# Kernel tuning notes

Hardware: AMD Instinct MI355X
Metric: run time of the kernel (lower is better)

Reference implementation:

```python
import jax, jax.numpy as jnp
import numpy as np

H, HKV, D, HID, INT = 16, 4, 128, 2048, 8192
ROPE_THETA = 10000.0
EPS = 1e-6
NEG = -1e30


def rmsnorm(x, w):
    v = jnp.mean(x * x, axis=-1, keepdims=True)
    return x * jax.lax.rsqrt(v + EPS) * w


def apply_rope(t, pos):
    # t: [B,S,h,D], pos: [S]
    half = D // 2
    inv_freq = 1.0 / (ROPE_THETA ** (jnp.arange(0, half, dtype=jnp.float32) / half))
    ang = pos.astype(jnp.float32)[:, None] * inv_freq  # [S, D/2]
    cos = jnp.cos(ang)[None, :, None, :]
    sin = jnp.sin(ang)[None, :, None, :]
    t1, t2 = t[..., :half], t[..., half:]
    return jnp.concatenate([t1 * cos - t2 * sin, t2 * cos + t1 * sin], axis=-1)


def setup_inputs() -> dict:
    key = jax.random.key(0)
    ks = jax.random.split(key, 5)
    B, S = 4, 1024
    s = 0.02  # init scale for weights
    return {
        "x": jax.random.normal(ks[0], (B, S, HID), jnp.float32),
        "ln1_w": jnp.ones((HID,), jnp.float32),
        "wqkv": jax.random.normal(ks[1], (HID, (H + 2 * HKV) * D), jnp.float32) * s,
        "wo": jax.random.normal(ks[2], (H * D, HID), jnp.float32) * s,
        "ln2_w": jnp.ones((HID,), jnp.float32),
        "w_gate_up": jax.random.normal(ks[3], (HID, 2 * INT), jnp.float32) * s,
        "w_down": jax.random.normal(ks[4], (INT, HID), jnp.float32) * s,
        "pos": jnp.arange(S, dtype=jnp.int32),
    }


def reference(x, ln1_w, wqkv, wo, ln2_w, w_gate_up, w_down, pos):
    B, S, _ = x.shape
    # --- attention block (prefill paged attention == dense causal attention) ---
    h = rmsnorm(x, ln1_w)
    qkv = h @ wqkv  # [B,S,(H+2*HKV)*D]
    q = qkv[..., : H * D].reshape(B, S, H, D)
    k = qkv[..., H * D : (H + HKV) * D].reshape(B, S, HKV, D)
    v = qkv[..., (H + HKV) * D :].reshape(B, S, HKV, D)
    q = apply_rope(q, pos)
    k = apply_rope(k, pos)
    g = H // HKV  # GQA group size
    k = jnp.repeat(k, g, axis=2)
    v = jnp.repeat(v, g, axis=2)
    scores = jnp.einsum("bqhd,bkhd->bhqk", q, k) / np.float32(np.sqrt(D))
    causal = pos[:, None] >= pos[None, :]  # [S,S]
    scores = jnp.where(causal[None, None], scores, NEG)
    attn = jax.nn.softmax(scores, axis=-1)
    o = jnp.einsum("bhqk,bkhd->bqhd", attn, v).reshape(B, S, H * D) @ wo
    h1 = x + o
    # --- SwiGLU MLP block ---
    gu = rmsnorm(h1, ln2_w) @ w_gate_up
    gate, up = gu[..., :INT], gu[..., INT:]
    return h1 + (jax.nn.silu(gate) * up) @ w_down
```

## Files before the change

### kernel.cpp

```cpp
#include <hip/hip_runtime.h>
#include <math.h>

#define B_    4
#define S_    1024
#define H_    16
#define HKV_  4
#define D_    128
#define HID_  2048
#define INT_  8192
#define QKVD_ 3072
#define NTOK_ 4096
#define NEG_  -1.0e30f

typedef unsigned short u16;
typedef unsigned int   u32;
typedef float  f32x4  __attribute__((ext_vector_type(4)));
typedef __bf16 bf16x8 __attribute__((ext_vector_type(8)));

__device__ __forceinline__ float bf2f(u16 v) {
    union { u32 u; float f; } c; c.u = ((u32)v) << 16; return c.f;
}
__device__ __forceinline__ u16 f2bf(float f) {
    union { float f; u32 u; } c; c.f = f;
    return (u16)((c.u + 0x7fffu + ((c.u >> 16) & 1u)) >> 16);
}

__device__ __forceinline__ void async_ld16(const u16* g, u16* l) {
    __builtin_amdgcn_global_load_lds(
        (const __attribute__((address_space(1))) void*)g,
        (__attribute__((address_space(3))) void*)l, 16, 0, 0);
}

__device__ __forceinline__ int swz_col(int e) {
    return ((((e >> 3) & 3) ^ ((e >> 5) & 3) ^ ((e >> 7) & 3)) << 3);
}

__device__ __forceinline__ void xcd2d(int gx, int gy, int RX, int RY,
                                      int& bx, int& by) {
    const int f = by * gx + bx;
    const int xcd = f & 7, slot = f >> 3;
    const int wx = gx / RX, wy = gy / RY;
    const int rx = xcd % RX, ry = xcd / RX;
    bx = rx * wx + (slot % wx);
    by = ry * wy + (slot / wx);
}

__global__ void detect_k(const u16* __restrict__ w, int* __restrict__ flag) {
    if (threadIdx.x == 0) *flag = (w[0] == 0x3F80u) ? 0 : 1;
}

__global__ void cvt_x_k(const void* __restrict__ in, const int* __restrict__ flag,
                        u16* __restrict__ out) {
    int i = blockIdx.x * 256 + threadIdx.x;
    if (*flag == 0) {
        ((ushort4*)out)[i] = ((const ushort4*)in)[i];
    } else {
        float4 v = ((const float4*)in)[i];
        ushort4 o;
        o.x = f2bf(v.x); o.y = f2bf(v.y); o.z = f2bf(v.z); o.w = f2bf(v.w);
        ((ushort4*)out)[i] = o;
    }
}

__global__ void cvt_w_k(const void* __restrict__ in, const int* __restrict__ flag,
                        float* __restrict__ out, int n) {
    int i = blockIdx.x * 256 + threadIdx.x;
    if (i < n) out[i] = (*flag == 0) ? bf2f(((const u16*)in)[i]) : ((const float*)in)[i];
}

__global__ void transpose_k(const void* __restrict__ in, const int* __restrict__ flag,
                            u16* __restrict__ out, int K, int N) {
    __shared__ u16 t[64][65];
    const bool isf32 = (*flag != 0);
    int tx = blockIdx.x * 64;
    int ty = blockIdx.y * 64;
    const int c4 = (threadIdx.x & 15) * 4;
    const int r0 = threadIdx.x >> 4;
    for (int r = r0; r < 64; r += 16) {
        size_t idx = (size_t)(ty + r) * N + tx + c4;
        if (isf32) {
            float4 v = *(const float4*)((const float*)in + idx);
            t[c4 + 0][r] = f2bf(v.x); t[c4 + 1][r] = f2bf(v.y);
            t[c4 + 2][r] = f2bf(v.z); t[c4 + 3][r] = f2bf(v.w);
        } else {
            ushort4 v = *(const ushort4*)((const u16*)in + idx);
            t[c4 + 0][r] = v.x; t[c4 + 1][r] = v.y;
            t[c4 + 2][r] = v.z; t[c4 + 3][r] = v.w;
        }
    }
    __syncthreads();
    for (int i = threadIdx.x; i < 64 * 16; i += 256) {
        int r = i >> 4, c = (i & 15) * 4;
        ushort4 v;
        v.x = t[r][c]; v.y = t[r][c + 1]; v.z = t[r][c + 2]; v.w = t[r][c + 3];
        *(ushort4*)(out + (size_t)(tx + r) * K + ty + c) = v;
    }
}

__global__ void rmsnorm_k(const u16* __restrict__ x, const float* __restrict__ w,
                          u16* __restrict__ y) {
    int row = blockIdx.x;
    const u16* xr = x + (size_t)row * HID_;
    u16* yr = y + (size_t)row * HID_;
    int t = threadIdx.x;
    u16 xs[8];
    *(uint4*)xs = ((const uint4*)xr)[t];
    float v[8]; float ss = 0.f;
    #pragma unroll
    for (int i = 0; i < 8; i++) { v[i] = bf2f(xs[i]); ss += v[i] * v[i]; }
    #pragma unroll
    for (int o = 32; o > 0; o >>= 1) ss += __shfl_down(ss, o, 64);
    __shared__ float wsum[4];
    if ((t & 63) == 0) wsum[t >> 6] = ss;
    __syncthreads();
    float tot = wsum[0] + wsum[1] + wsum[2] + wsum[3];
    float scale = rsqrtf(tot * (1.0f / HID_) + 1e-6f);
    float4 w0 = ((const float4*)w)[t * 2];
    float4 w1 = ((const float4*)w)[t * 2 + 1];
    float wf[8] = {w0.x, w0.y, w0.z, w0.w, w1.x, w1.y, w1.z, w1.w};
    u16 ys[8];
    #pragma unroll
    for (int i = 0; i < 8; i++) ys[i] = f2bf(v[i] * scale * wf[i]);
    ((uint4*)yr)[t] = *(uint4*)ys;
}

__global__ void rope_table_k(const int* __restrict__ pos,
                             float* __restrict__ cosT, float* __restrict__ sinT) {
    int s = blockIdx.x;
    int d = threadIdx.x;
    double inv = exp(-((double)d / 64.0) * 9.210340371976184);
    double ang = (double)pos[s] * inv;
    cosT[s * 64 + d] = (float)cos(ang);
    sinT[s * 64 + d] = (float)sin(ang);
}

__global__ void rope_apply_k(u16* __restrict__ qkv, const float* __restrict__ cosT,
                             const float* __restrict__ sinT) {
    int id = blockIdx.x * 256 + threadIdx.x;
    int d4 = (id & 15) * 4;
    int rest = id >> 4;
    int head = rest % 20;
    int bs = rest / 20;
    int s = bs & (S_ - 1);
    size_t base = (size_t)bs * QKVD_ + head * D_;
    ushort4 lo = *(ushort4*)(qkv + base + d4);
    ushort4 hi = *(ushort4*)(qkv + base + 64 + d4);
    float4 c  = *(const float4*)(cosT + s * 64 + d4);
    float4 sn = *(const float4*)(sinT + s * 64 + d4);
    float t1[4] = {bf2f(lo.x), bf2f(lo.y), bf2f(lo.z), bf2f(lo.w)};
    float t2[4] = {bf2f(hi.x), bf2f(hi.y), bf2f(hi.z), bf2f(hi.w)};
    float cf[4] = {c.x, c.y, c.z, c.w};
    float sf[4] = {sn.x, sn.y, sn.z, sn.w};
    ushort4 olo, ohi;
    olo.x = f2bf(t1[0] * cf[0] - t2[0] * sf[0]);
    olo.y = f2bf(t1[1] * cf[1] - t2[1] * sf[1]);
    olo.z = f2bf(t1[2] * cf[2] - t2[2] * sf[2]);
    olo.w = f2bf(t1[3] * cf[3] - t2[3] * sf[3]);
    ohi.x = f2bf(t2[0] * cf[0] + t1[0] * sf[0]);
    ohi.y = f2bf(t2[1] * cf[1] + t1[1] * sf[1]);
    ohi.z = f2bf(t2[2] * cf[2] + t1[2] * sf[2]);
    ohi.w = f2bf(t2[3] * cf[3] + t1[3] * sf[3]);
    *(ushort4*)(qkv + base + d4)      = olo;
    *(ushort4*)(qkv + base + 64 + d4) = ohi;
}

template<int EPI>
__global__ __launch_bounds__(512, 2) void gemm256_k(
    const u16* __restrict__ A, const u16* __restrict__ Bt,
    void* __restrict__ Cv, int M, int N, int K, int RX, int RY)
{
    __shared__ __align__(16) u16 lds[3 * 16384];

    int bx = blockIdx.x, by = blockIdx.y;
    xcd2d(gridDim.x, gridDim.y, RX, RY, bx, by);

    const int tid  = threadIdx.x;
    const int m0 = by * 256, n0 = bx * 256;
    const int wave = tid >> 6, lane = tid & 63;
    const int wmi = wave >> 2, wni = wave & 3;
    const int r16 = lane & 15, quad = lane >> 4;

    const int NT = K >> 5;

    auto stageA = [&](int bufi, int tt) {
        u16* dst = lds + bufi * 16384;
        const size_t gb = (size_t)m0 * K + (size_t)tt * 32;
        #pragma unroll
        for (int rr = 0; rr < 2; ++rr) {
            const int e = rr * 4096 + tid * 8;
            async_ld16(A + gb + (size_t)(e >> 5) * K + swz_col(e), dst + e);
        }
    };
    auto stageB = [&](int bufi, int tt) {
        u16* dst = lds + bufi * 16384 + 8192;
        const size_t gb = (size_t)n0 * K + (size_t)tt * 32;
        #pragma unroll
        for (int rr = 0; rr < 2; ++rr) {
            const int e = rr * 4096 + tid * 8;
            async_ld16(Bt + gb + (size_t)(e >> 5) * K + swz_col(e), dst + e);
        }
    };

    f32x4 acc[8][4] = {};

    stageA(0, 0); stageB(0, 0);
    stageA(1, 1); stageB(1, 1);
    asm volatile("s_waitcnt vmcnt(4)" ::: "memory");
    __builtin_amdgcn_s_barrier();

    const int gsw = quad ^ (r16 & 3) ^ ((r16 >> 2) & 3);
    const int aoff = wmi * 4096 + r16 * 32 + gsw * 8;
    const int boff = 8192 + wni * 2048 + r16 * 32 + gsw * 8;

    for (int t = 0; t < NT; ++t) {
        const u16* buf = lds + (t % 3) * 16384;
        const int nb = (t + 2) % 3;
        const bool pf = (t + 2) < NT;
        bf16x8 a[4], b[4], a2[4];
        #pragma unroll
        for (int i = 0; i < 4; ++i) a[i] = *(const bf16x8*)(buf + aoff + i * 512);
        #pragma unroll
        for (int j = 0; j < 4; ++j) b[j] = *(const bf16x8*)(buf + boff + j * 512);
        if (pf) stageA(nb, t + 2);
        __builtin_amdgcn_s_barrier();
        asm volatile("s_waitcnt lgkmcnt(0)" ::: "memory");
        __builtin_amdgcn_sched_barrier(0);
        __builtin_amdgcn_s_setprio(1);
        #pragma unroll
        for (int i = 0; i < 4; ++i)
            #pragma unroll
            for (int j = 0; j < 4; ++j)
                acc[i][j] = __builtin_amdgcn_mfma_f32_16x16x32_bf16(a[i], b[j], acc[i][j], 0, 0, 0);
        __builtin_amdgcn_s_setprio(0);
        __builtin_amdgcn_s_barrier();
        #pragma unroll
        for (int i = 0; i < 4; ++i) a2[i] = *(const bf16x8*)(buf + aoff + (i + 4) * 512);
        if (pf) stageB(nb, t + 2);
        __builtin_amdgcn_s_barrier();
        asm volatile("s_waitcnt lgkmcnt(0)" ::: "memory");
        __builtin_amdgcn_sched_barrier(0);
        __builtin_amdgcn_s_setprio(1);
        #pragma unroll
        for (int i = 0; i < 4; ++i)
            #pragma unroll
            for (int j = 0; j < 4; ++j)
                acc[i + 4][j] = __builtin_amdgcn_mfma_f32_16x16x32_bf16(a2[i], b[j], acc[i + 4][j], 0, 0, 0);
        __builtin_amdgcn_s_setprio(0);
        if (t == NT - 2) { asm volatile("s_waitcnt vmcnt(0)" ::: "memory"); }
        else             { asm volatile("s_waitcnt vmcnt(4)" ::: "memory"); }
        __builtin_amdgcn_s_barrier();
    }

    u16* C16 = (u16*)Cv;
    #pragma unroll
    for (int i = 0; i < 8; ++i) {
        const int mb = m0 + wmi * 128 + i * 16 + quad * 4;
        #pragma unroll
        for (int j = 0; j < 4; ++j) {
            const int n = n0 + wni * 64 + j * 16 + r16;
            #pragma unroll
            for (int r = 0; r < 4; ++r) {
                size_t idx = (size_t)(mb + r) * N + n;
                float v = acc[i][j][r];
                if (EPI == 2) { v = v / (1.f + __expf(-v)); v *= bf2f(C16[idx]); }
                C16[idx] = f2bf(v);
            }
        }
    }
}

template<int EPI>
__global__ __launch_bounds__(512, 2) void gemm_bt2_k(
    const u16* __restrict__ A, const u16* __restrict__ Bt,
    void* __restrict__ Cv, const u16* __restrict__ R,
    const int* __restrict__ flag, int M, int N, int K, int RX, int RY)
{
    __shared__ __align__(16) u16 lds[3 * 12288];

    int bx = blockIdx.x, by = blockIdx.y;
    xcd2d(gridDim.x, gridDim.y, RX, RY, bx, by);

    const int tid  = threadIdx.x;
    const int m0 = by * 128, n0 = bx * 256;
    const int wave = tid >> 6, lane = tid & 63;
    const int wmi = wave >> 2, wni = wave & 3;
    const int r16 = lane & 15, quad = lane >> 4;

    const int NT = K >> 5;

    auto stageA = [&](int bufi, int tt) {
        u16* dst = lds + bufi * 12288;
        const size_t gb = (size_t)m0 * K + (size_t)tt * 32;
        const int e = tid * 8;
        async_ld16(A + gb + (size_t)(e >> 5) * K + swz_col(e), dst + e);
    };
    auto stageB = [&](int bufi, int tt) {
        u16* dst = lds + bufi * 12288 + 4096;
        const size_t gb = (size_t)n0 * K + (size_t)tt * 32;
        #pragma unroll
        for (int rr = 0; rr < 2; ++rr) {
            const int e = rr * 4096 + tid * 8;
            async_ld16(Bt + gb + (size_t)(e >> 5) * K + swz_col(e), dst + e);
        }
    };

    f32x4 acc[4][4] = {};

    stageA(0, 0); stageB(0, 0);
    stageA(1, 1); stageB(1, 1);
    asm volatile("s_waitcnt vmcnt(3)" ::: "memory");
    __builtin_amdgcn_s_barrier();

    const int gsw = quad ^ (r16 & 3) ^ ((r16 >> 2) & 3);
    const int aoff = wmi * 2048 + r16 * 32 + gsw * 8;
    const int boff = 4096 + wni * 2048 + r16 * 32 + gsw * 8;

    for (int t = 0; t < NT; ++t) {
        const u16* buf = lds + (t % 3) * 12288;
        const int nb = (t + 2) % 3;
        const bool pf = (t + 2) < NT;
        bf16x8 a[4], b2[2], b3[2];
        #pragma unroll
        for (int i = 0; i < 4; ++i) a[i] = *(const bf16x8*)(buf + aoff + i * 512);
        #pragma unroll
        for (int j = 0; j < 2; ++j) b2[j] = *(const bf16x8*)(buf + boff + j * 512);
        if (pf) stageA(nb, t + 2);
        __builtin_amdgcn_s_barrier();
        asm volatile("s_waitcnt lgkmcnt(0)" ::: "memory");
        __builtin_amdgcn_sched_barrier(0);
        __builtin_amdgcn_s_setprio(1);
        #pragma unroll
        for (int i = 0; i < 4; ++i)
            #pragma unroll
            for (int j = 0; j < 2; ++j)
                acc[i][j] = __builtin_amdgcn_mfma_f32_16x16x32_bf16(a[i], b2[j], acc[i][j], 0, 0, 0);
        __builtin_amdgcn_s_setprio(0);
        __builtin_amdgcn_s_barrier();
        #pragma unroll
        for (int j = 0; j < 2; ++j) b3[j] = *(const bf16x8*)(buf + boff + (j + 2) * 512);
        if (pf) stageB(nb, t + 2);
        __builtin_amdgcn_s_barrier();
        asm volatile("s_waitcnt lgkmcnt(0)" ::: "memory");
        __builtin_amdgcn_sched_barrier(0);
        __builtin_amdgcn_s_setprio(1);
        #pragma unroll
        for (int i = 0; i < 4; ++i)
            #pragma unroll
            for (int j = 0; j < 2; ++j)
                acc[i][j + 2] = __builtin_amdgcn_mfma_f32_16x16x32_bf16(a[i], b3[j], acc[i][j + 2], 0, 0, 0);
        __builtin_amdgcn_s_setprio(0);
        if (t == NT - 2) { asm volatile("s_waitcnt vmcnt(0)" ::: "memory"); }
        else             { asm volatile("s_waitcnt vmcnt(3)" ::: "memory"); }
        __builtin_amdgcn_s_barrier();
    }

    u16* C16 = (u16*)Cv;
    float* C32 = (float*)Cv;
    bool f32out = false;
    if (EPI == 3) f32out = (*flag != 0);

    #pragma unroll
    for (int i = 0; i < 4; ++i) {
        const int mb = m0 + wmi * 64 + i * 16 + quad * 4;
        #pragma unroll
        for (int j = 0; j < 4; ++j) {
            const int n = n0 + wni * 64 + j * 16 + r16;
            #pragma unroll
            for (int r = 0; r < 4; ++r) {
                size_t idx = (size_t)(mb + r) * N + n;
                float v = acc[i][j][r];
                v += bf2f(R[idx]);
                if (EPI == 3 && f32out) C32[idx] = v;
                else C16[idx] = f2bf(v);
            }
        }
    }
}

__global__ __launch_bounds__(256) void attn_mfma_k(
    const u16* __restrict__ qkv, u16* __restrict__ out)
{
    __shared__ __align__(16) u16 Vt[128 * 136];
    __shared__ __align__(16) u16 Ps[64 * 136];

    int bswz_x, bswz_y, bswz_z;
    {
        const int orig = blockIdx.x + (S_ / 64) * (blockIdx.y + H_ * blockIdx.z);
        const int q = ((S_ / 64) * H_ * B_) >> 3;
        const int wg = (orig & 7) * q + (orig >> 3);
        bswz_x = wg & (S_ / 64 - 1);
        bswz_y = (wg >> 4) & (H_ - 1);
        bswz_z = wg >> 8;
    }

    const int tid  = threadIdx.x;
    const int wave = tid >> 6, lane = tid & 63;
    const int r16  = lane & 15, quad = lane >> 4;
    const int q0 = bswz_x * 64;
    const int h  = bswz_y;
    const int b  = bswz_z;
    const int kh = h >> 2;
    const float scale = 0.08838834764831845f;

    bf16x8 a_q[4];
    {
        const u16* qp = qkv + ((size_t)(b * S_ + q0 + wave * 16 + r16) * QKVD_ + h * D_ + quad * 8);
        #pragma unroll
        for (int ks = 0; ks < 4; ks++)
            a_q[ks] = *(const bf16x8*)(qp + ks * 32);
    }

    float mrun[4], lrun[4];
    #pragma unroll
    for (int r = 0; r < 4; r++) { mrun[r] = -3.0e38f; lrun[r] = 0.f; }
    f32x4 acc_o[8] = {};
    const int myrow_c = q0 + wave * 16 + quad * 4;

    const int ntiles = (q0 >> 7) + 1;
    for (int kt = 0; kt < ntiles; kt++) {
        const int j0 = kt * 128;
        __syncthreads();
        {
            const int key = tid & 127, dh = (tid >> 7) * 64;
            const u16* vp = qkv + ((size_t)(b * S_ + j0 + key) * QKVD_ + (H_ + HKV_ + kh) * D_ + dh);
            #pragma unroll
            for (int i = 0; i < 8; i++) {
                u16 tmp[8];
                *(uint4*)tmp = *(const uint4*)(vp + i * 8);
                #pragma unroll
                for (int j = 0; j < 8; j++)
                    Vt[(dh + i * 8 + j) * 136 + key] = tmp[j];
            }
        }
        f32x4 acc_s[8] = {};
        __builtin_amdgcn_s_setprio(1);
        #pragma unroll
        for (int ks = 0; ks < 4; ks++) {
            #pragma unroll
            for (int nt = 0; nt < 8; nt++) {
                const u16* kp = qkv + ((size_t)(b * S_ + j0 + nt * 16 + r16) * QKVD_
                                       + (H_ + kh) * D_ + ks * 32 + quad * 8);
                bf16x8 bk = *(const bf16x8*)kp;
                acc_s[nt] = __builtin_amdgcn_mfma_f32_16x16x32_bf16(a_q[ks], bk, acc_s[nt], 0, 0, 0);
            }
        }
        __builtin_amdgcn_s_setprio(0);
        const bool lastt = (kt == ntiles - 1);
        float mnew[4];
        #pragma unroll
        for (int r = 0; r < 4; r++) mnew[r] = mrun[r];
        #pragma unroll
        for (int nt = 0; nt < 8; nt++) {
            const int col = j0 + nt * 16 + r16;
            #pragma unroll
            for (int r = 0; r < 4; r++) {
                float v = acc_s[nt][r] * scale;
                if (lastt && col > myrow_c + r) v = NEG_;
                acc_s[nt][r] = v;
                mnew[r] = fmaxf(mnew[r], v);
            }
        }
        #pragma unroll
        for (int o = 1; o < 16; o <<= 1)
            #pragma unroll
            for (int r = 0; r < 4; r++)
                mnew[r] = fmaxf(mnew[r], __shfl_xor(mnew[r], o, 64));
        float alpha[4], lsum[4];
        #pragma unroll
        for (int r = 0; r < 4; r++) {
            alpha[r] = __expf(mrun[r] - mnew[r]);
            mrun[r] = mnew[r];
            lsum[r] = 0.f;
        }
        #pragma unroll
        for (int nt = 0; nt < 8; nt++) {
            #pragma unroll
            for (int r = 0; r < 4; r++) {
                float p = __expf(acc_s[nt][r] - mrun[r]);
                lsum[r] += p;
                Ps[(wave * 16 + quad * 4 + r) * 136 + nt * 16 + r16] = f2bf(p);
            }
        }
        #pragma unroll
        for (int o = 1; o < 16; o <<= 1)
            #pragma unroll
            for (int r = 0; r < 4; r++)
                lsum[r] += __shfl_xor(lsum[r], o, 64);
        #pragma unroll
        for (int r = 0; r < 4; r++) lrun[r] = lrun[r] * alpha[r] + lsum[r];
        #pragma unroll
        for (int nt = 0; nt < 8; nt++)
            #pragma unroll
            for (int r = 0; r < 4; r++) acc_o[nt][r] *= alpha[r];
        __syncthreads();
        __builtin_amdgcn_s_setprio(1);
        #pragma unroll
        for (int ks = 0; ks < 4; ks++) {
            bf16x8 ap = *(const bf16x8*)(Ps + (wave * 16 + r16) * 136 + ks * 32 + quad * 8);
            #pragma unroll
            for (int nt = 0; nt < 8; nt++) {
                bf16x8 bv = *(const bf16x8*)(Vt + (nt * 16 + r16) * 136 + ks * 32 + quad * 8);
                acc_o[nt] = __builtin_amdgcn_mfma_f32_16x16x32_bf16(ap, bv, acc_o[nt], 0, 0, 0);
            }
        }
        __builtin_amdgcn_s_setprio(0);
    }
    #pragma unroll
    for (int r = 0; r < 4; r++) {
        const float linv = 1.0f / lrun[r];
        const int tok = myrow_c + r;
        u16* orow = out + ((size_t)(b * S_ + tok) * (H_ * D_) + h * D_ + r16);
        #pragma unroll
        for (int nt = 0; nt < 8; nt++)
            orow[nt * 16] = f2bf(acc_o[nt][r] * linv);
    }
}

extern "C" void kernel_launch(void* const* d_in, const int* in_sizes, int n_in,
                              void* d_out, int out_size, void* d_ws, size_t ws_size,
                              hipStream_t stream)
{
    const void* x    = d_in[0];
    const u16*  ln1w = (const u16*)d_in[1];
    const void* wqkv = d_in[2];
    const void* wo   = d_in[3];
    const void* ln2w = d_in[4];
    const void* wgu  = d_in[5];
    const void* wd   = d_in[6];
    const int*  pos  = (const int*)d_in[7];

    char* wsb = (char*)d_ws;
    size_t off = 0;
    auto alloc = [&](size_t bytes) {
        char* p = wsb + off; off = (off + bytes + 255) & ~(size_t)255; return p;
    };
    int*  flag  = (int*)alloc(256);
    u16*  xb    = (u16*)alloc(2ull * NTOK_ * HID_);
    float* wln1 = (float*)alloc(4ull * HID_);
    float* wln2 = (float*)alloc(4ull * HID_);
    u16* wqkvT = (u16*)alloc(2ull * 3072 * 2048);
    u16* woT   = (u16*)alloc(2ull * 2048 * 2048);
    u16* wguT  = (u16*)alloc(2ull * 16384 * 2048);
    u16* wdT   = (u16*)alloc(2ull * 2048 * 8192);
    u16* h     = (u16*)alloc(2ull * NTOK_ * HID_);
    u16* qkv   = (u16*)alloc(2ull * NTOK_ * QKVD_);
    u16* h1    = (u16*)alloc(2ull * NTOK_ * HID_);
    u16* su    = (u16*)alloc(2ull * NTOK_ * INT_);
    float* cosT = (float*)alloc(4ull * S_ * 64);
    float* sinT = (float*)alloc(4ull * S_ * 64);
    u16* attn_out = h;
    u16* mlp_in   = qkv;

    detect_k<<<1, 64, 0, stream>>>(ln1w, flag);

    cvt_x_k<<<(NTOK_ * HID_ / 4 + 255) / 256, 256, 0, stream>>>(x, flag, xb);
    cvt_w_k<<<8, 256, 0, stream>>>(d_in[1], flag, wln1, HID_);
    cvt_w_k<<<8, 256, 0, stream>>>(ln2w, flag, wln2, HID_);

    transpose_k<<<dim3(3072 / 64, 2048 / 64), 256, 0, stream>>>(wqkv, flag, wqkvT, 2048, 3072);
    transpose_k<<<dim3(2048 / 64, 2048 / 64), 256, 0, stream>>>(wo, flag, woT, 2048, 2048);
    transpose_k<<<dim3(16384 / 64, 2048 / 64), 256, 0, stream>>>(wgu, flag, wguT, 2048, 16384);
    transpose_k<<<dim3(2048 / 64, 8192 / 64), 256, 0, stream>>>(wd, flag, wdT, 8192, 2048);

    rope_table_k<<<S_, 64, 0, stream>>>(pos, cosT, sinT);

    rmsnorm_k<<<NTOK_, 256, 0, stream>>>(xb, wln1, h);
    gemm256_k<0><<<dim3(3072 / 256, NTOK_ / 256), 512, 0, stream>>>(
        h, wqkvT, qkv, NTOK_, QKVD_, HID_, 2, 4);
    rope_apply_k<<<(NTOK_ * 20 * 16) / 256, 256, 0, stream>>>(qkv, cosT, sinT);
    attn_mfma_k<<<dim3(S_ / 64, H_, B_), 256, 0, stream>>>(qkv, attn_out);
    gemm_bt2_k<1><<<dim3(2048 / 256, NTOK_ / 128), 512, 0, stream>>>(
        attn_out, woT, h1, xb, nullptr, NTOK_, HID_, HID_, 2, 4);
    rmsnorm_k<<<NTOK_, 256, 0, stream>>>(h1, wln2, mlp_in);
    gemm256_k<0><<<dim3(8192 / 256, NTOK_ / 256), 512, 0, stream>>>(
        mlp_in, wguT + (size_t)8192 * 2048, su, NTOK_, INT_, HID_, 4, 2);
    gemm256_k<2><<<dim3(8192 / 256, NTOK_ / 256), 512, 0, stream>>>(
        mlp_in, wguT, su, NTOK_, INT_, HID_, 4, 2);
    gemm_bt2_k<3><<<dim3(2048 / 256, NTOK_ / 128), 512, 0, stream>>>(
        su, wdT, d_out, h1, flag, NTOK_, HID_, INT_, 2, 4);
}
```

Before: 1.085 ms.

## Switch GEMM kernels from triple to double-buffered LDS with one barrier per tile

Both bf16 GEMM kernels move from a 3-stage LDS ring with prefetch distance 2 and several barriers per K-tile to a 2-stage ping-pong buffer. The next tile's A and B loads are issued at the top of each iteration, and all LDS fragment reads are issued before a split lgkmcnt wait. Only one vmcnt(0) wait and one barrier remain per tile. This cuts LDS footprint and barrier count, which may help occupancy. The cost is a shorter prefetch distance, so global-load latency is hidden behind only one tile of MFMA work.

```diff
diff --git a/kernel.cpp b/kernel.cpp
--- a/kernel.cpp
+++ b/kernel.cpp
@@ -169,7 +169,7 @@
     const u16* __restrict__ A, const u16* __restrict__ Bt,
     void* __restrict__ Cv, int M, int N, int K, int RX, int RY)
 {
-    __shared__ __align__(16) u16 lds[3 * 16384];
+    __shared__ __align__(16) u16 lds[2 * 16384];
 
     int bx = blockIdx.x, by = blockIdx.y;
     xcd2d(gridDim.x, gridDim.y, RX, RY, bx, by);
@@ -204,8 +204,7 @@
     f32x4 acc[8][4] = {};
 
     stageA(0, 0); stageB(0, 0);
-    stageA(1, 1); stageB(1, 1);
-    asm volatile("s_waitcnt vmcnt(4)" ::: "memory");
+    asm volatile("s_waitcnt vmcnt(0)" ::: "memory");
     __builtin_amdgcn_s_barrier();
 
     const int gsw = quad ^ (r16 & 3) ^ ((r16 >> 2) & 3);
@@ -213,16 +212,25 @@
     const int boff = 8192 + wni * 2048 + r16 * 32 + gsw * 8;
 
     for (int t = 0; t < NT; ++t) {
-        const u16* buf = lds + (t % 3) * 16384;
-        const int nb = (t + 2) % 3;
-        const bool pf = (t + 2) < NT;
+        const u16* buf = lds + (t & 1) * 16384;
+        const int nb = (t & 1) ^ 1;
+        if (t + 1 < NT) { stageA(nb, t + 1); stageB(nb, t + 1); }
         bf16x8 a[4], b[4], a2[4];
         #pragma unroll
         for (int i = 0; i < 4; ++i) a[i] = *(const bf16x8*)(buf + aoff + i * 512);
         #pragma unroll
         for (int j = 0; j < 4; ++j) b[j] = *(const bf16x8*)(buf + boff + j * 512);
-        if (pf) stageA(nb, t + 2);
-        __builtin_amdgcn_s_barrier();
+        #pragma unroll
+        for (int i = 0; i < 4; ++i) a2[i] = *(const bf16x8*)(buf + aoff + (i + 4) * 512);
+        asm volatile("s_waitcnt lgkmcnt(4)" ::: "memory");
+        __builtin_amdgcn_sched_barrier(0);
+        __builtin_amdgcn_s_setprio(1);
+        #pragma unroll
+        for (int i = 0; i < 4; ++i)
+            #pragma unroll
+            for (int j = 0; j < 4; ++j)
+                acc[i][j] = __builtin_amdgcn_mfma_f32_16x16x32_bf16(a[i], b[j], acc[i][j], 0, 0, 0);
+        __builtin_amdgcn_s_setprio(0);
         asm volatile("s_waitcnt lgkmcnt(0)" ::: "memory");
         __builtin_amdgcn_sched_barrier(0);
         __builtin_amdgcn_s_setprio(1);
@@ -230,24 +238,9 @@
         for (int i = 0; i < 4; ++i)
             #pragma unroll
             for (int j = 0; j < 4; ++j)
-                acc[i][j] = __builtin_amdgcn_mfma_f32_16x16x32_bf16(a[i], b[j], acc[i][j], 0, 0, 0);
-        __builtin_amdgcn_s_setprio(0);
-        __builtin_amdgcn_s_barrier();
-        #pragma unroll
-        for (int i = 0; i < 4; ++i) a2[i] = *(const bf16x8*)(buf + aoff + (i + 4) * 512);
-        if (pf) stageB(nb, t + 2);
-        __builtin_amdgcn_s_barrier();
-        asm volatile("s_waitcnt lgkmcnt(0)" ::: "memory");
-        __builtin_amdgcn_sched_barrier(0);
-        __builtin_amdgcn_s_setprio(1);
-        #pragma unroll
-        for (int i = 0; i < 4; ++i)
-            #pragma unroll
-            for (int j = 0; j < 4; ++j)
                 acc[i + 4][j] = __builtin_amdgcn_mfma_f32_16x16x32_bf16(a2[i], b[j], acc[i + 4][j], 0, 0, 0);
         __builtin_amdgcn_s_setprio(0);
-        if (t == NT - 2) { asm volatile("s_waitcnt vmcnt(0)" ::: "memory"); }
-        else             { asm volatile("s_waitcnt vmcnt(4)" ::: "memory"); }
+        asm volatile("s_waitcnt vmcnt(0)" ::: "memory");
         __builtin_amdgcn_s_barrier();
     }
 
@@ -275,7 +268,7 @@
     void* __restrict__ Cv, const u16* __restrict__ R,
     const int* __restrict__ flag, int M, int N, int K, int RX, int RY)
 {
-    __shared__ __align__(16) u16 lds[3 * 12288];
+    __shared__ __align__(16) u16 lds[2 * 12288];
 
     int bx = blockIdx.x, by = blockIdx.y;
     xcd2d(gridDim.x, gridDim.y, RX, RY, bx, by);
@@ -307,8 +300,7 @@
     f32x4 acc[4][4] = {};
 
     stageA(0, 0); stageB(0, 0);
-    stageA(1, 1); stageB(1, 1);
-    asm volatile("s_waitcnt vmcnt(3)" ::: "memory");
+    asm volatile("s_waitcnt vmcnt(0)" ::: "memory");
     __builtin_amdgcn_s_barrier();
 
     const int gsw = quad ^ (r16 & 3) ^ ((r16 >> 2) & 3);
@@ -316,16 +308,25 @@
     const int boff = 4096 + wni * 2048 + r16 * 32 + gsw * 8;
 
     for (int t = 0; t < NT; ++t) {
-        const u16* buf = lds + (t % 3) * 12288;
-        const int nb = (t + 2) % 3;
-        const bool pf = (t + 2) < NT;
+        const u16* buf = lds + (t & 1) * 12288;
+        const int nb = (t & 1) ^ 1;
+        if (t + 1 < NT) { stageA(nb, t + 1); stageB(nb, t + 1); }
         bf16x8 a[4], b2[2], b3[2];
         #pragma unroll
         for (int i = 0; i < 4; ++i) a[i] = *(const bf16x8*)(buf + aoff + i * 512);
         #pragma unroll
         for (int j = 0; j < 2; ++j) b2[j] = *(const bf16x8*)(buf + boff + j * 512);
-        if (pf) stageA(nb, t + 2);
-        __builtin_amdgcn_s_barrier();
+        #pragma unroll
+        for (int j = 0; j < 2; ++j) b3[j] = *(const bf16x8*)(buf + boff + (j + 2) * 512);
+        asm volatile("s_waitcnt lgkmcnt(2)" ::: "memory");
+        __builtin_amdgcn_sched_barrier(0);
+        __builtin_amdgcn_s_setprio(1);
+        #pragma unroll
+        for (int i = 0; i < 4; ++i)
+            #pragma unroll
+            for (int j = 0; j < 2; ++j)
+                acc[i][j] = __builtin_amdgcn_mfma_f32_16x16x32_bf16(a[i], b2[j], acc[i][j], 0, 0, 0);
+        __builtin_amdgcn_s_setprio(0);
         asm volatile("s_waitcnt lgkmcnt(0)" ::: "memory");
         __builtin_amdgcn_sched_barrier(0);
         __builtin_amdgcn_s_setprio(1);
@@ -333,24 +334,9 @@
         for (int i = 0; i < 4; ++i)
             #pragma unroll
             for (int j = 0; j < 2; ++j)
-                acc[i][j] = __builtin_amdgcn_mfma_f32_16x16x32_bf16(a[i], b2[j], acc[i][j], 0, 0, 0);
-        __builtin_amdgcn_s_setprio(0);
-        __builtin_amdgcn_s_barrier();
-        #pragma unroll
-        for (int j = 0; j < 2; ++j) b3[j] = *(const bf16x8*)(buf + boff + (j + 2) * 512);
-        if (pf) stageB(nb, t + 2);
-        __builtin_amdgcn_s_barrier();
-        asm volatile("s_waitcnt lgkmcnt(0)" ::: "memory");
-        __builtin_amdgcn_sched_barrier(0);
-        __builtin_amdgcn_s_setprio(1);
-        #pragma unroll
-        for (int i = 0; i < 4; ++i)
-            #pragma unroll
-            for (int j = 0; j < 2; ++j)
                 acc[i][j + 2] = __builtin_amdgcn_mfma_f32_16x16x32_bf16(a[i], b3[j], acc[i][j + 2], 0, 0, 0);
         __builtin_amdgcn_s_setprio(0);
-        if (t == NT - 2) { asm volatile("s_waitcnt vmcnt(0)" ::: "memory"); }
-        else             { asm volatile("s_waitcnt vmcnt(3)" ::: "memory"); }
+        asm volatile("s_waitcnt vmcnt(0)" ::: "memory");
         __builtin_amdgcn_s_barrier();
     }
 
```

Measured after the change: 1.111 ms. 1.02x slower.
